# Optimization experiments

Hardware: AMD Instinct MI355X
Metric: run time of the kernel (lower is better)

The kernel has to match this reference:

```python
import jax, jax.numpy as jnp
import numpy as np

B, N, D, H = 4, 1024, 256, 8  # batch, seq, in_dim(=per-head qkv_dim), n_heads


def setup_inputs() -> dict:
    key = jax.random.key(0)
    k1, k2, k3 = jax.random.split(key, 3)
    x = jax.random.normal(k1, (B, N, D), dtype=jnp.float32)
    Wqkv = jax.random.normal(k2, (D, 3 * D * H), dtype=jnp.float32) * 0.02
    bqkv = jnp.zeros((3 * D * H,), dtype=jnp.float32)
    W0 = jax.random.normal(k3, (D * H, D), dtype=jnp.float32) * 0.02
    b0 = jnp.zeros((D,), dtype=jnp.float32)
    return {"x": x, "Wqkv": Wqkv, "bqkv": bqkv, "W0": W0, "b0": b0}


def reference(x, Wqkv, bqkv, W0, b0):
    b, n, d = x.shape
    h = Wqkv.shape[1] // (3 * d)
    qkv = x @ Wqkv + bqkv                      # [b, n, 3*d*h]
    # Faithful to torch: raw row-major reinterpretation of the buffer.
    q, k, v = jnp.reshape(qkv, (3, b, n, d, h))
    score = jnp.einsum('bnqh,btqh->bnth', q, k) * (d ** -0.5)  # [b, n, n, h]
    attn = jax.nn.softmax(score, axis=1)       # softmax over query axis (dim=1), as in source
    # einsum 'bnnh,bnqh->bnqh' = diagonal of attn times v (faithful to source)
    av = jnp.einsum('bnnh,bnqh->bnqh', attn, v)  # [b, n, d, h]
    out = av.reshape(b, n, d * h) @ W0 + b0    # [b, n, d]
    return out
```

## Files before the change

### kernel.cpp

```cpp
#include <hip/hip_runtime.h>


#define SEGSZ 8388608

typedef short v8s __attribute__((ext_vector_type(8)));
typedef float v4f __attribute__((ext_vector_type(4)));

__device__ __forceinline__ ushort f2bf(float v) {
  union { float f; unsigned u; } x; x.f = v;
  const unsigned r = x.u + 0x7fff + ((x.u >> 16) & 1);
  return (ushort)(r >> 16);
}
__device__ __forceinline__ float bf2f(ushort v) {
  union { unsigned u; float f; } x; x.u = ((unsigned)v) << 16;
  return x.f;
}

#define GLOAD_LDS16(g, l)                                            \
  __builtin_amdgcn_global_load_lds(                                  \
      (const __attribute__((address_space(1))) void*)(g),            \
      (__attribute__((address_space(3))) void*)(l), 16, 0, 0)

#define SBAR()   asm volatile("s_barrier" ::: "memory")
#define VMCNT4() asm volatile("s_waitcnt vmcnt(4)" ::: "memory")
#define VMCNT0() asm volatile("s_waitcnt vmcnt(0)" ::: "memory")

__global__ __launch_bounds__(256) void prep(
    const float* __restrict__ X, const float* __restrict__ Wqkv,
    const float* __restrict__ W0, ushort* __restrict__ xb,
    ushort* __restrict__ whT, ushort* __restrict__ w0T) {
  __shared__ float T[64][65];
  const int tid = threadIdx.x;
  int bid = blockIdx.x;

  if (bid < 1024) {
    const size_t i = ((size_t)bid * 256 + tid) * 4;
    const float4 v = *(const float4*)&X[i];
    ushort4 hv = {f2bf(v.x), f2bf(v.y), f2bf(v.z), f2bf(v.w)};
    *(ushort4*)&xb[i] = hv;
    return;
  }
  bid -= 1024;
  if (bid < 384) {
    const int n0 = (bid % 96) * 64;
    const int k0 = (bid / 96) * 64;
    {
      const int row = tid >> 2;
      const int c0 = (tid & 3) * 16;
#pragma unroll
      for (int j = 0; j < 16; j += 4) {
        const float4 v = *(const float4*)&Wqkv[(size_t)(k0 + row) * 6144 + n0 + c0 + j];
        T[row][c0 + j + 0] = v.x; T[row][c0 + j + 1] = v.y;
        T[row][c0 + j + 2] = v.z; T[row][c0 + j + 3] = v.w;
      }
    }
    __syncthreads();
    {
      const int nn = tid >> 2;
      const int kk0 = (tid & 3) * 16;
      const int n = n0 + nn;
      const int seg = n >> 11, h = n & 7, d = (n & 2047) >> 3;
      const int p = seg * 2048 + h * 256 + d;
      ushort hv[16];
#pragma unroll
      for (int j = 0; j < 16; ++j) hv[j] = f2bf(T[kk0 + j][nn]);
      const size_t base = (size_t)p * 256 + k0 + kk0;
#pragma unroll
      for (int j = 0; j < 16; j += 8) *(v8s*)&whT[base + j] = *(v8s*)&hv[j];
    }
    return;
  }
  bid -= 384;
  {
    const int e0 = (bid & 3) * 64;
    const int k0 = (bid >> 2) * 64;
    {
      const int row = tid >> 2;
      const int c0 = (tid & 3) * 16;
#pragma unroll
      for (int j = 0; j < 16; j += 4) {
        const float4 v = *(const float4*)&W0[(size_t)(k0 + row) * 256 + e0 + c0 + j];
        T[row][c0 + j + 0] = v.x; T[row][c0 + j + 1] = v.y;
        T[row][c0 + j + 2] = v.z; T[row][c0 + j + 3] = v.w;
      }
    }
    __syncthreads();
    {
      const int ee = tid >> 2;
      const int kk0 = (tid & 3) * 16;
#pragma unroll
      for (int j = 0; j < 16; ++j) {
        const int k = k0 + kk0 + j;
        const int d = k >> 3, h = k & 7;
        w0T[(size_t)(e0 + ee) * 2048 + h * 256 + d] = f2bf(T[kk0 + j][ee]);
      }
    }
  }
}

template <int STRIDE>
__device__ __forceinline__ void gemm256_8ph(
    const ushort* __restrict__ gA, const ushort* __restrict__ gB,
    ushort (&AS)[2][16384], ushort (&BS)[2][16384],
    v4f (&acc)[2][2][4][2]) {
  const int tid = threadIdx.x;
  const int wave = tid >> 6, lane = tid & 63;
  const int wm = wave >> 2, wn = wave & 3;
  const int quad = lane >> 4, l15 = lane & 15;
  const int srow = lane >> 3;
  const int scol = (((lane & 7) ^ srow) << 3);

  auto stage = [&](int op, int buf, int half, int kt) {
#pragma unroll
    for (int j = 0; j < 2; ++j) {
      const size_t grow =
          (size_t)(half * 128 + j * 64 + wave * 8 + srow) * STRIDE + kt * 64 + scol;
      ushort* lb = op ? &BS[buf][half * 8192 + j * 4096 + wave * 512]
                      : &AS[buf][half * 8192 + j * 4096 + wave * 512];
      GLOAD_LDS16((op ? gB : gA) + grow, lb);
    }
  };

  stage(0, 0, 0, 0); stage(0, 0, 1, 0); stage(1, 0, 0, 0); stage(1, 0, 1, 0);
  stage(0, 1, 0, 1); stage(1, 1, 0, 1);
  VMCNT4();
  SBAR();

#pragma unroll
  for (int it = 0; it < 2; ++it) {
    const int t0 = it * 2;
#pragma unroll
    for (int p = 0; p < 8; ++p) {
      const int kb = p >> 2;
      const int qr = (p >> 1) & 1, qc = p & 1;
      v8s af[4][2], bfr[2][2];
#pragma unroll
      for (int ri = 0; ri < 4; ++ri) {
        const int r = qr * 128 + wm * 64 + ri * 16 + l15;
        const int rx = r & 7;
#pragma unroll
        for (int ks = 0; ks < 2; ++ks)
          af[ri][ks] = *(const v8s*)&AS[kb][r * 64 + ((((ks << 2) | quad) ^ rx) << 3)];
      }
#pragma unroll
      for (int ci = 0; ci < 2; ++ci) {
        const int r = qc * 128 + wn * 32 + ci * 16 + l15;
        const int rx = r & 7;
#pragma unroll
        for (int ks = 0; ks < 2; ++ks)
          bfr[ci][ks] = *(const v8s*)&BS[kb][r * 64 + ((((ks << 2) | quad) ^ rx) << 3)];
      }
      {
        const int st = t0 + 1 + ((p + 2) >> 2);
        if (st < 4) stage(p & 1, st & 1, 1 - ((p >> 1) & 1), st);
      }
      SBAR();
      __builtin_amdgcn_s_setprio(1);
#pragma unroll
      for (int ri = 0; ri < 4; ++ri)
#pragma unroll
        for (int ci = 0; ci < 2; ++ci)
#pragma unroll
          for (int ks = 0; ks < 2; ++ks)
            acc[qr][qc][ri][ci] = __builtin_amdgcn_mfma_f32_16x16x32_bf16(
                af[ri][ks], bfr[ci][ks], acc[qr][qc][ri][ci], 0, 0, 0);
      __builtin_amdgcn_s_setprio(0);
      if (p == 3 || p == 7) { if (it == 0) VMCNT4(); else VMCNT0(); }
      SBAR();
    }
  }
}

__global__ __launch_bounds__(512, 2) void qkv8(
    const ushort* __restrict__ xb, const ushort* __restrict__ whT,
    const float* __restrict__ bias, ushort* __restrict__ qkvb) {
  __shared__ ushort AS[2][16384];
  __shared__ ushort BS[2][16384];
  const int tid = threadIdx.x;
  const int wave = tid >> 6, lane = tid & 63;
  const int wm = wave >> 2, wn = wave & 3;
  const int quad = lane >> 4, l15 = lane & 15;
  const int c0 = blockIdx.x * 256;
  const int r0 = blockIdx.y * 256;

  v4f acc[2][2][4][2] = {};
  gemm256_8ph<256>(xb + (size_t)r0 * 256, whT + (size_t)c0 * 256, AS, BS, acc);

#pragma unroll
  for (int qc2 = 0; qc2 < 2; ++qc2)
#pragma unroll
    for (int ci = 0; ci < 2; ++ci) {
      const int cc = c0 + qc2 * 128 + wn * 32 + ci * 16 + l15;
      const int cseg = cc >> 11;
      const int hh = (cc & 2047) >> 8;
      const int d = cc & 255;
      const float bv = bias[cseg * 2048 + d * 8 + hh];
#pragma unroll
      for (int qr = 0; qr < 2; ++qr)
#pragma unroll
        for (int ri = 0; ri < 4; ++ri)
#pragma unroll
          for (int rg = 0; rg < 4; ++rg) {
            const int r = r0 + qr * 128 + wm * 64 + ri * 16 + quad * 4 + rg;
            const int g = r * 3 + cseg;
            const int seg = g >> 12;
            const int tok = g & 4095;
            float val = acc[qr][qc2][ri][ci][rg] + bv;
            if (seg == 0) val *= 0.0625f;
            qkvb[(size_t)seg * SEGSZ + (size_t)tok * 2048 + hh * 256 + d] = f2bf(val);
          }
    }
}

__global__ __launch_bounds__(512, 2) void mid8(
    const ushort* __restrict__ qkvb, const ushort* __restrict__ w0T,
    float* __restrict__ pl, float* __restrict__ sd_ws,
    ushort* __restrict__ partial) {
  __shared__ ushort AS[2][16384];
  __shared__ ushort BS[2][16384];
  __shared__ float redL[2][4][64];
  const int tid = threadIdx.x;
  const int wave = tid >> 6, lane = tid & 63;
  const int wm = wave >> 2, wn = wave & 3;
  const int quad = lane >> 4, l15 = lane & 15;
  const int id = blockIdx.x;

  v4f acc[2][2][4][2] = {};

  if (id < 512) {
    const int c = id & 7, inner = id >> 3;
    const int bh = (inner >> 4) * 8 + c;
    const int tile = inner & 15;
    const int tt0 = (tile >> 2) * 256;
    const int nn0 = (tile & 3) * 256;
    const int b = bh >> 3, h = bh & 7;
    const ushort* Qg = qkvb + (size_t)b * 2097152 + h * 256 + (size_t)nn0 * 2048;
    const ushort* Kg = qkvb + SEGSZ + (size_t)b * 2097152 + h * 256 + (size_t)tt0 * 2048;
    gemm256_8ph<2048>(Qg, Kg, AS, BS, acc);

    float lsum[2][2];
#pragma unroll
    for (int qc2 = 0; qc2 < 2; ++qc2)
#pragma unroll
      for (int ci = 0; ci < 2; ++ci) {
        float s = 0.f;
#pragma unroll
        for (int qr = 0; qr < 2; ++qr)
#pragma unroll
          for (int ri = 0; ri < 4; ++ri)
#pragma unroll
            for (int rg = 0; rg < 4; ++rg)
              s += __expf(acc[qr][qc2][ri][ci][rg]);
        s += __shfl_xor(s, 16, 64);
        s += __shfl_xor(s, 32, 64);
        lsum[qc2][ci] = s;
      }
    if (quad == 0) {
#pragma unroll
      for (int qc2 = 0; qc2 < 2; ++qc2)
#pragma unroll
        for (int ci = 0; ci < 2; ++ci)
          redL[wm][wn][(qc2 * 2 + ci) * 16 + l15] = lsum[qc2][ci];
    }
    __syncthreads();
    if (wm == 0 && quad == 0) {
#pragma unroll
      for (int qc2 = 0; qc2 < 2; ++qc2)
#pragma unroll
        for (int ci = 0; ci < 2; ++ci) {
          const int t = tt0 + qc2 * 128 + wn * 32 + ci * 16 + l15;
          const float l = lsum[qc2][ci] + redL[1][wn][(qc2 * 2 + ci) * 16 + l15];
          pl[((size_t)bh * 1024 + t) * 4 + (nn0 >> 8)] = l;
        }
    }

    if (tt0 == nn0) {
#pragma unroll
      for (int qr = 0; qr < 2; ++qr)
#pragma unroll
        for (int ci = 0; ci < 2; ++ci)
#pragma unroll
          for (int ri = 0; ri < 4; ++ri)
#pragma unroll
            for (int rg = 0; rg < 4; ++rg)
              if (wn * 2 + ci - wm * 4 == ri && (l15 >> 2) == quad &&
                  (l15 & 3) == rg) {
                const int t = tt0 + qr * 128 + wm * 64 + ri * 16 + l15;
                sd_ws[(size_t)bh * 1024 + t] = acc[qr][qr][ri][ci][rg];
              }
    }
  } else {
    const int j = id - 512;
    const int h = j >> 4;
    const int tok0 = (j & 15) * 256;
    const ushort* Ag = qkvb + 2 * (size_t)SEGSZ + (size_t)tok0 * 2048 + h * 256;
    const ushort* Bg = w0T + h * 256;
    gemm256_8ph<2048>(Ag, Bg, AS, BS, acc);

#pragma unroll
    for (int qr = 0; qr < 2; ++qr)
#pragma unroll
      for (int ri = 0; ri < 4; ++ri)
#pragma unroll
        for (int rg = 0; rg < 4; ++rg) {
          const int tok = tok0 + qr * 128 + wm * 64 + ri * 16 + quad * 4 + rg;
#pragma unroll
          for (int qc2 = 0; qc2 < 2; ++qc2)
#pragma unroll
            for (int ci = 0; ci < 2; ++ci) {
              const int e = qc2 * 128 + wn * 32 + ci * 16 + l15;
              partial[(size_t)h * 1048576 + (size_t)tok * 256 + e] =
                  f2bf(acc[qr][qc2][ri][ci][rg]);
            }
        }
  }
}

__global__ __launch_bounds__(256) void av_atomic(
    const ushort* __restrict__ vb, const ushort* __restrict__ w0T,
    const float* __restrict__ pl, const float* __restrict__ sd,
    float* __restrict__ out) {
  __shared__ ushort As[128 * 32];
  __shared__ ushort Bs[128 * 32];
  __shared__ float diagS[128];
  const int tid = threadIdx.x;
  const int wave = tid >> 6, lane = tid & 63;
  const int quad = lane >> 4, l15 = lane & 15;
  const int e0 = blockIdx.x * 128;
  const int tok0 = blockIdx.y * 128;
  const int h = blockIdx.z;
  const int kbase = h * 256;
  const int wr = (wave >> 1) * 64;
  const int wc = (wave & 1) * 64;

  if (tid < 128) {
    const int bh = (tok0 >> 10) * 8 + h;
    const int t = (tok0 & 1023) + tid;
    const size_t base = ((size_t)bh * 1024 + t) * 4;
    float l = 0.f;
#pragma unroll
    for (int cc = 0; cc < 4; ++cc) l += pl[base + cc];
    diagS[tid] = __expf(sd[(size_t)bh * 1024 + t]) / l;
  }

  v4f acc[4][4] = {};

  for (int d0 = 0; d0 < 256; d0 += 32) {
#pragma unroll
    for (int half = 0; half < 2; ++half) {
      const int rr = wave * 32 + half * 16;
      const int row = rr + (lane >> 2);
      const int gcol = kbase + d0 + (lane & 3) * 8;
      GLOAD_LDS16(vb + (size_t)(tok0 + row) * 2048 + gcol, &As[rr * 32]);
      GLOAD_LDS16(w0T + (size_t)(e0 + row) * 2048 + gcol, &Bs[rr * 32]);
    }
    __syncthreads();

    v8s aF[4], bF[4];
#pragma unroll
    for (int i = 0; i < 4; ++i) {
      aF[i] = *(const v8s*)&As[(wr + i * 16 + l15) * 32 + quad * 8];
      bF[i] = *(const v8s*)&Bs[(wc + i * 16 + l15) * 32 + quad * 8];
    }
#pragma unroll
    for (int ri = 0; ri < 4; ++ri)
#pragma unroll
      for (int ci = 0; ci < 4; ++ci)
        acc[ri][ci] =
            __builtin_amdgcn_mfma_f32_16x16x32_bf16(aF[ri], bF[ci], acc[ri][ci], 0, 0, 0);
    __syncthreads();
  }

#pragma unroll
  for (int ri = 0; ri < 4; ++ri)
#pragma unroll
    for (int rg = 0; rg < 4; ++rg) {
      const int lrow = wr + ri * 16 + quad * 4 + rg;
      const int tok = tok0 + lrow;
      const float dg = diagS[lrow];
#pragma unroll
      for (int ci = 0; ci < 4; ++ci) {
        const int e = e0 + wc + ci * 16 + l15;
        atomicAdd(&out[(size_t)tok * 256 + e], acc[ri][ci][rg] * dg);
      }
    }
}

__global__ void init_out(const float* __restrict__ b0, float* __restrict__ out) {
  const int i = blockIdx.x * 256 + threadIdx.x;
  const int e0 = (i & 63) << 2;
  *(float4*)&out[(size_t)i * 4] = *(const float4*)&b0[e0];
}

__global__ void reduce_out(const ushort* __restrict__ partial,
                           const float* __restrict__ pl,
                           const float* __restrict__ sd,
                           const float* __restrict__ b0, float* __restrict__ out) {
  __shared__ float dgS[32];
  const int i = blockIdx.x * 256 + threadIdx.x;
  const int tbase = blockIdx.x * 4;
  if (threadIdx.x < 32) {
    const int tl = threadIdx.x >> 3, h = threadIdx.x & 7;
    const int tok = tbase + tl;
    const int bh = (tok >> 10) * 8 + h;
    const int t = tok & 1023;
    const size_t base = ((size_t)bh * 1024 + t) * 4;
    float l = 0.f;
#pragma unroll
    for (int cc = 0; cc < 4; ++cc) l += pl[base + cc];
    dgS[threadIdx.x] = __expf(sd[(size_t)bh * 1024 + t]) / l;
  }
  __syncthreads();
  const int tl = threadIdx.x >> 6;
  const int e0 = (i & 63) << 2;
  float4 a = *(const float4*)&b0[e0];
#pragma unroll
  for (int h = 0; h < 8; ++h) {
    const float dg = dgS[tl * 8 + h];
    const ushort4 p = *(const ushort4*)&partial[(size_t)h * 1048576 + (size_t)i * 4];
    a.x += dg * bf2f(p.x); a.y += dg * bf2f(p.y);
    a.z += dg * bf2f(p.z); a.w += dg * bf2f(p.w);
  }
  *(float4*)&out[(size_t)i * 4] = a;
}

extern "C" void kernel_launch(void* const* d_in, const int* in_sizes, int n_in,
                              void* d_out, int out_size, void* d_ws, size_t ws_size,
                              hipStream_t stream) {
  const float* x    = (const float*)d_in[0];
  const float* Wqkv = (const float*)d_in[1];
  const float* bqkv = (const float*)d_in[2];
  const float* W0   = (const float*)d_in[3];
  const float* b0   = (const float*)d_in[4];
  float* out = (float*)d_out;

  float*  pl   = (float*)d_ws;
  float*  sd   = pl + 262144;
  ushort* qkvb = (ushort*)(sd + 32768);
  ushort* xb   = qkvb + 3 * (size_t)SEGSZ;
  ushort* whT  = xb + 1048576;
  ushort* w0T  = whT + 1572864;
  ushort* partial = w0T + 524288;

  ushort* vb = qkvb + 2 * (size_t)SEGSZ;

  const size_t need_base =
      (size_t)(262144 + 32768) * 4 + (size_t)SEGSZ * 3 * 2 +
      (size_t)(1048576 + 1572864 + 524288) * 2;
  const bool full = ws_size >= need_base + (size_t)8 * 1048576 * 2;

  prep<<<1536, 256, 0, stream>>>(x, Wqkv, W0, xb, whT, w0T);
  qkv8<<<dim3(24, 16), 512, 0, stream>>>(xb, whT, bqkv, qkvb);
  if (full) {
    mid8<<<640, 512, 0, stream>>>(qkvb, w0T, pl, sd, partial);
    reduce_out<<<1024, 256, 0, stream>>>(partial, pl, sd, b0, out);
  } else {
    mid8<<<512, 512, 0, stream>>>(qkvb, w0T, pl, sd, nullptr);
    init_out<<<1024, 256, 0, stream>>>(b0, out);
    av_atomic<<<dim3(2, 32, 8), 256, 0, stream>>>(vb, w0T, pl, sd, out);
  }
}
```

Before: 142.2 us.

## Replace double-buffered 8-phase GEMM pipeline with single-buffer loop for higher occupancy

```diff
diff --git a/kernel.cpp b/kernel.cpp
--- a/kernel.cpp
+++ b/kernel.cpp
@@ -22,7 +22,6 @@
       (__attribute__((address_space(3))) void*)(l), 16, 0, 0)
 
 #define SBAR()   asm volatile("s_barrier" ::: "memory")
-#define VMCNT4() asm volatile("s_waitcnt vmcnt(4)" ::: "memory")
 #define VMCNT0() asm volatile("s_waitcnt vmcnt(0)" ::: "memory")
 
 __global__ __launch_bounds__(256) void prep(
@@ -99,9 +98,9 @@
 }
 
 template <int STRIDE>
-__device__ __forceinline__ void gemm256_8ph(
+__device__ __forceinline__ void gemm256_sb(
     const ushort* __restrict__ gA, const ushort* __restrict__ gB,
-    ushort (&AS)[2][16384], ushort (&BS)[2][16384],
+    ushort (&AS)[16384], ushort (&BS)[16384],
     v4f (&acc)[2][2][4][2]) {
   const int tid = threadIdx.x;
   const int wave = tid >> 6, lane = tid & 63;
@@ -110,72 +109,62 @@
   const int srow = lane >> 3;
   const int scol = (((lane & 7) ^ srow) << 3);
 
-  auto stage = [&](int op, int buf, int half, int kt) {
-#pragma unroll
-    for (int j = 0; j < 2; ++j) {
+  auto stage = [&](int kt) {
+#pragma unroll
+    for (int j = 0; j < 4; ++j) {
       const size_t grow =
-          (size_t)(half * 128 + j * 64 + wave * 8 + srow) * STRIDE + kt * 64 + scol;
-      ushort* lb = op ? &BS[buf][half * 8192 + j * 4096 + wave * 512]
-                      : &AS[buf][half * 8192 + j * 4096 + wave * 512];
-      GLOAD_LDS16((op ? gB : gA) + grow, lb);
+          (size_t)(j * 64 + wave * 8 + srow) * STRIDE + kt * 64 + scol;
+      GLOAD_LDS16(gA + grow, &AS[j * 4096 + wave * 512]);
+      GLOAD_LDS16(gB + grow, &BS[j * 4096 + wave * 512]);
     }
   };
 
-  stage(0, 0, 0, 0); stage(0, 0, 1, 0); stage(1, 0, 0, 0); stage(1, 0, 1, 0);
-  stage(0, 1, 0, 1); stage(1, 1, 0, 1);
-  VMCNT4();
-  SBAR();
-
-#pragma unroll
-  for (int it = 0; it < 2; ++it) {
-    const int t0 = it * 2;
-#pragma unroll
-    for (int p = 0; p < 8; ++p) {
-      const int kb = p >> 2;
-      const int qr = (p >> 1) & 1, qc = p & 1;
-      v8s af[4][2], bfr[2][2];
+#pragma unroll
+  for (int kt = 0; kt < 4; ++kt) {
+    stage(kt);
+    VMCNT0();
+    SBAR();
+#pragma unroll
+    for (int qr = 0; qr < 2; ++qr) {
+      v8s af[4][2];
 #pragma unroll
       for (int ri = 0; ri < 4; ++ri) {
         const int r = qr * 128 + wm * 64 + ri * 16 + l15;
         const int rx = r & 7;
 #pragma unroll
         for (int ks = 0; ks < 2; ++ks)
-          af[ri][ks] = *(const v8s*)&AS[kb][r * 64 + ((((ks << 2) | quad) ^ rx) << 3)];
-      }
-#pragma unroll
-      for (int ci = 0; ci < 2; ++ci) {
-        const int r = qc * 128 + wn * 32 + ci * 16 + l15;
-        const int rx = r & 7;
-#pragma unroll
-        for (int ks = 0; ks < 2; ++ks)
-          bfr[ci][ks] = *(const v8s*)&BS[kb][r * 64 + ((((ks << 2) | quad) ^ rx) << 3)];
-      }
-      {
-        const int st = t0 + 1 + ((p + 2) >> 2);
-        if (st < 4) stage(p & 1, st & 1, 1 - ((p >> 1) & 1), st);
-      }
-      SBAR();
-      __builtin_amdgcn_s_setprio(1);
-#pragma unroll
-      for (int ri = 0; ri < 4; ++ri)
-#pragma unroll
-        for (int ci = 0; ci < 2; ++ci)
+          af[ri][ks] = *(const v8s*)&AS[r * 64 + ((((ks << 2) | quad) ^ rx) << 3)];
+      }
+#pragma unroll
+      for (int qc = 0; qc < 2; ++qc) {
+        v8s bfr[2][2];
+#pragma unroll
+        for (int ci = 0; ci < 2; ++ci) {
+          const int r = qc * 128 + wn * 32 + ci * 16 + l15;
+          const int rx = r & 7;
 #pragma unroll
           for (int ks = 0; ks < 2; ++ks)
-            acc[qr][qc][ri][ci] = __builtin_amdgcn_mfma_f32_16x16x32_bf16(
-                af[ri][ks], bfr[ci][ks], acc[qr][qc][ri][ci], 0, 0, 0);
-      __builtin_amdgcn_s_setprio(0);
-      if (p == 3 || p == 7) { if (it == 0) VMCNT4(); else VMCNT0(); }
-      SBAR();
-    }
-  }
-}
-
-__global__ __launch_bounds__(512, 2) void qkv8(
+            bfr[ci][ks] = *(const v8s*)&BS[r * 64 + ((((ks << 2) | quad) ^ rx) << 3)];
+        }
+#pragma unroll
+        for (int ri = 0; ri < 4; ++ri)
+#pragma unroll
+          for (int ci = 0; ci < 2; ++ci)
+#pragma unroll
+            for (int ks = 0; ks < 2; ++ks)
+              acc[qr][qc][ri][ci] = __builtin_amdgcn_mfma_f32_16x16x32_bf16(
+                  af[ri][ks], bfr[ci][ks], acc[qr][qc][ri][ci], 0, 0, 0);
+      }
+    }
+    SBAR();
+  }
+}
+
+__global__ __launch_bounds__(512, 4) void qkv8(
     const ushort* __restrict__ xb, const ushort* __restrict__ whT,
     const float* __restrict__ bias, ushort* __restrict__ qkvb) {
-  __shared__ ushort AS[2][16384];
-  __shared__ ushort BS[2][16384];
+  __shared__ ushort AS[16384];
+  __shared__ ushort BS[16384];
   const int tid = threadIdx.x;
   const int wave = tid >> 6, lane = tid & 63;
   const int wm = wave >> 2, wn = wave & 3;
@@ -184,7 +173,7 @@
   const int r0 = blockIdx.y * 256;
 
   v4f acc[2][2][4][2] = {};
-  gemm256_8ph<256>(xb + (size_t)r0 * 256, whT + (size_t)c0 * 256, AS, BS, acc);
+  gemm256_sb<256>(xb + (size_t)r0 * 256, whT + (size_t)c0 * 256, AS, BS, acc);
 
 #pragma unroll
   for (int qc2 = 0; qc2 < 2; ++qc2)
@@ -212,12 +201,12 @@
     }
 }
 
-__global__ __launch_bounds__(512, 2) void mid8(
+__global__ __launch_bounds__(512, 4) void mid8(
     const ushort* __restrict__ qkvb, const ushort* __restrict__ w0T,
     float* __restrict__ pl, float* __restrict__ sd_ws,
     ushort* __restrict__ partial) {
-  __shared__ ushort AS[2][16384];
-  __shared__ ushort BS[2][16384];
+  __shared__ ushort AS[16384];
+  __shared__ ushort BS[16384];
   __shared__ float redL[2][4][64];
   const int tid = threadIdx.x;
   const int wave = tid >> 6, lane = tid & 63;
@@ -236,7 +225,7 @@
     const int b = bh >> 3, h = bh & 7;
     const ushort* Qg = qkvb + (size_t)b * 2097152 + h * 256 + (size_t)nn0 * 2048;
     const ushort* Kg = qkvb + SEGSZ + (size_t)b * 2097152 + h * 256 + (size_t)tt0 * 2048;
-    gemm256_8ph<2048>(Qg, Kg, AS, BS, acc);
+    gemm256_sb<2048>(Qg, Kg, AS, BS, acc);
 
     float lsum[2][2];
 #pragma unroll
@@ -295,7 +284,7 @@
     const int tok0 = (j & 15) * 256;
     const ushort* Ag = qkvb + 2 * (size_t)SEGSZ + (size_t)tok0 * 2048 + h * 256;
     const ushort* Bg = w0T + h * 256;
-    gemm256_8ph<2048>(Ag, Bg, AS, BS, acc);
+    gemm256_sb<2048>(Ag, Bg, AS, BS, acc);
 
 #pragma unroll
     for (int qr = 0; qr < 2; ++qr)
```

After: 344.4 us. 142% more time.
